# Kernel tuning notes

Measured on AMD Instinct MI355X. Metric: run time of the kernel, lower is better.

The kernel has to match this reference:

```python
import jax, jax.numpy as jnp
import numpy as np
from jax import lax

B, S, NX, NSFC, H, NY = 8192, 64, 4, 5, 32, 1


def _lstm(x, h0, c0, w_ih, w_hh, b_ih, b_hh):
    """batch_first LSTM, PyTorch gate order (i, f, g, o).
    x: [B,S,I]; h0,c0: [B,H]; w_ih: [4H,I]; w_hh: [4H,H]. Returns [B,S,H]."""
    # Precompute the input projection for all timesteps (big GEMM, once).
    xg = jnp.einsum('bsi,gi->bsg', x, w_ih) + b_ih + b_hh  # [B,S,4H]

    def step(carry, xg_t):
        h, c = carry
        gates = xg_t + h @ w_hh.T  # [B,4H]
        i, f, g, o = jnp.split(gates, 4, axis=-1)
        i = jax.nn.sigmoid(i)
        f = jax.nn.sigmoid(f)
        g = jnp.tanh(g)
        o = jax.nn.sigmoid(o)
        c = f * c + i * g
        h = o * jnp.tanh(c)
        return (h, c), h

    (_, _), hs = lax.scan(step, (h0, c0), jnp.swapaxes(xg, 0, 1))  # hs: [S,B,H]
    return jnp.swapaxes(hs, 0, 1)


def setup_inputs() -> dict:
    key = jax.random.key(0)
    ks = jax.random.split(key, 16)
    s = 1.0 / np.sqrt(H)

    def u(k, shape):
        return jax.random.uniform(k, shape, jnp.float32, -s, s)

    return {
        'inputs_main': jax.random.normal(ks[0], (B, S, NX), jnp.float32),
        'inputs_sfc': jax.random.normal(ks[1], (B, NSFC), jnp.float32),
        'w_sfc1': u(ks[2], (H, NSFC)), 'b_sfc1': u(ks[3], (H,)),
        'w_sfc2': u(ks[4], (H, NSFC)), 'b_sfc2': u(ks[5], (H,)),
        'w_ih1': u(ks[6], (4 * H, NX)), 'w_hh1': u(ks[7], (4 * H, H)),
        'b_ih1': u(ks[8], (4 * H,)), 'b_hh1': u(ks[9], (4 * H,)),
        'w_ih2': u(ks[10], (4 * H, H)), 'w_hh2': u(ks[11], (4 * H, H)),
        'b_ih2': u(ks[12], (4 * H,)), 'b_hh2': u(ks[13], (4 * H,)),
        'w_out': u(ks[14], (NY, H)), 'b_out': u(ks[15], (NY,)),
    }


def reference(inputs_main, inputs_sfc,
              w_sfc1, b_sfc1, w_sfc2, b_sfc2,
              w_ih1, w_hh1, b_ih1, b_hh1,
              w_ih2, w_hh2, b_ih2, b_hh2,
              w_out, b_out):
    # Surface MLPs -> initial (h0, c0) of rnn1
    h0 = jnp.tanh(inputs_sfc @ w_sfc1.T + b_sfc1)  # [B,H]
    c0 = jnp.tanh(inputs_sfc @ w_sfc2.T + b_sfc2)  # [B,H]

    # rnn1 runs on time-reversed input; its output is flipped back
    x = jnp.flip(inputs_main, axis=1)
    out = _lstm(x, h0, c0, w_ih1, w_hh1, b_ih1, b_hh1)
    out = jnp.flip(out, axis=1)

    # rnn2 with zero initial state (PyTorch default)
    z = jnp.zeros((out.shape[0], H), out.dtype)
    out2 = _lstm(out, z, z, w_ih2, w_hh2, b_ih2, b_hh2)

    # Output MLP (concat=False -> last layer output only)
    return out2 @ w_out.T + b_out  # [B,S,NY]
```

## Files before the change

kernel.cpp:

```cpp
#include <hip/hip_runtime.h>

typedef __attribute__((ext_vector_type(4))) float f32x4;
typedef __attribute__((ext_vector_type(8))) short bf16x8;

#define LOG2E 1.44269504088896340736f

__device__ __forceinline__ float bcf(unsigned u){ union{unsigned u;float f;}v; v.u=u; return v.f; }
__device__ __forceinline__ unsigned pkbf(float a, float b){
    unsigned w; asm("v_cvt_pk_bf16_f32 %0, %1, %2" : "=v"(w) : "v"(a), "v"(b)); return w;
}
__device__ __forceinline__ float ex2(float x){ return __builtin_amdgcn_exp2f(x); }
__device__ __forceinline__ float rcp_(float x){ return __builtin_amdgcn_rcpf(x); }

#define MFMA(a,b,c) __builtin_amdgcn_mfma_f32_16x16x32_bf16(a,b,c,0,0,0)

union FragU { unsigned w[4]; bf16x8 v; };

__device__ __forceinline__ void split8(const float* v, bf16x8 &fh, bf16x8 &fl){
    FragU H, L;
#pragma unroll
    for (int i=0;i<4;i++){
        unsigned w = pkbf(v[2*i], v[2*i+1]);
        H.w[i] = w;
        float ra = v[2*i]   - bcf(w<<16);
        float rb = v[2*i+1] - bcf(w & 0xffff0000u);
        L.w[i] = pkbf(ra, rb);
    }
    fh = H.v; fl = L.v;
}

__device__ __forceinline__ void build_bx(const float4& x, int hi, FragU& B){
    unsigned w0 = pkbf(x.x, x.y), w1 = pkbf(x.z, x.w);
    float r0 = x.x - bcf(w0<<16), r1 = x.y - bcf(w0 & 0xffff0000u);
    float r2 = x.z - bcf(w1<<16), r3 = x.w - bcf(w1 & 0xffff0000u);
    unsigned l0 = pkbf(r0,r1), l1 = pkbf(r2,r3);
    const bool h01 = (hi < 2);
    B.w[0] = h01 ? w0 : 0u;
    B.w[1] = h01 ? w1 : 0u;
    B.w[2] = (hi==0) ? l0 : (hi==1 ? 0x3f803f80u : 0u);
    B.w[3] = (hi==0) ? l1 : 0u;
}

__device__ __forceinline__ void write_h(unsigned (*hb)[16][20], int b15, int hi, int wv_,
                                        const float* hv){
    unsigned h0 = pkbf(hv[0], hv[1]);
    unsigned h1 = pkbf(hv[2], hv[3]);
    float r0 = hv[0]-bcf(h0<<16), r1 = hv[1]-bcf(h0 & 0xffff0000u);
    float r2 = hv[2]-bcf(h1<<16), r3 = hv[3]-bcf(h1 & 0xffff0000u);
    unsigned l0 = pkbf(r0,r1), l1 = pkbf(r2,r3);
    const int wi = 8*wv_ + 2*hi;
    *(uint2*)&hb[0][b15][wi] = make_uint2(h0,h1);
    *(uint2*)&hb[1][b15][wi] = make_uint2(l0,l1);
}

__global__ __launch_bounds__(128) void lstm2_mfma2(
    const float* __restrict__ xin,
    const float* __restrict__ sfc,
    const float* __restrict__ w_sfc1, const float* __restrict__ b_sfc1,
    const float* __restrict__ w_sfc2, const float* __restrict__ b_sfc2,
    const float* __restrict__ w_ih1, const float* __restrict__ w_hh1,
    const float* __restrict__ b_ih1, const float* __restrict__ b_hh1,
    const float* __restrict__ w_ih2, const float* __restrict__ w_hh2,
    const float* __restrict__ b_ih2, const float* __restrict__ b_hh2,
    const float* __restrict__ w_out, const float* __restrict__ b_out,
    float* __restrict__ outp)
{
    __shared__ __align__(16) unsigned out1q[64][16][16];
    __shared__ __align__(16) unsigned hbuf[2][2][16][20];
    __shared__ float ybuf[2][64][16];

    const int tid  = threadIdx.x;
    const int wv   = tid >> 6;
    const int lane = tid & 63;
    const int b15  = lane & 15;
    const int hi   = (lane >> 4) & 3;
    const int B0   = blockIdx.x * 16;

    bf16x8 Whh_h[4], Whh_l[4], WxA[4];
    bf16x8 W2h_h[4], W2h_l[4], W2x_h[4], W2x_l[4];
    float bia[4][4], woutr[4];
#pragma unroll
    for (int c=0;c<4;c++){
        const int gr = 32*c + 16*wv + b15;
        const float sc = (c==2) ? (2.0f*LOG2E) : (-LOG2E);
        float wvv[8];
        {
            float4 wa = *(const float4*)(w_hh1 + gr*32 + 8*hi);
            float4 wb = *(const float4*)(w_hh1 + gr*32 + 8*hi + 4);
            wvv[0]=wa.x*sc; wvv[1]=wa.y*sc; wvv[2]=wa.z*sc; wvv[3]=wa.w*sc;
            wvv[4]=wb.x*sc; wvv[5]=wb.y*sc; wvv[6]=wb.z*sc; wvv[7]=wb.w*sc;
        }
        split8(wvv, Whh_h[c], Whh_l[c]);
        {
            float4 wi = *(const float4*)(w_ih1 + gr*4);
            float wh0=wi.x*sc, wh1=wi.y*sc, wh2=wi.z*sc, wh3=wi.w*sc;
            unsigned xw0 = pkbf(wh0,wh1), xw1 = pkbf(wh2,wh3);
            float wl0 = wh0-bcf(xw0<<16), wl1 = wh1-bcf(xw0 & 0xffff0000u);
            float wl2 = wh2-bcf(xw1<<16), wl3 = wh3-bcf(xw1 & 0xffff0000u);
            unsigned lw0 = pkbf(wl0,wl1), lw1 = pkbf(wl2,wl3);
            float bias = (b_ih1[gr] + b_hh1[gr])*sc;
            unsigned bh = pkbf(bias, 0.0f);
            float blo = bias - bcf(bh<<16);
            unsigned bword = pkbf(bias, blo);
            FragU A;
            if (hi==0){ A.w[0]=xw0; A.w[1]=xw1; A.w[2]=xw0; A.w[3]=xw1; }
            else if (hi==1){ A.w[0]=lw0; A.w[1]=lw1; A.w[2]=bword; A.w[3]=0u; }
            else { A.w[0]=0u; A.w[1]=0u; A.w[2]=0u; A.w[3]=0u; }
            WxA[c] = A.v;
        }
        {
            float4 wa = *(const float4*)(w_hh2 + gr*32 + 8*hi);
            float4 wb = *(const float4*)(w_hh2 + gr*32 + 8*hi + 4);
            wvv[0]=wa.x*sc; wvv[1]=wa.y*sc; wvv[2]=wa.z*sc; wvv[3]=wa.w*sc;
            wvv[4]=wb.x*sc; wvv[5]=wb.y*sc; wvv[6]=wb.z*sc; wvv[7]=wb.w*sc;
        }
        split8(wvv, W2h_h[c], W2h_l[c]);
        {
            const float scx = sc * (1.0f/32767.0f);
            float4 wa = *(const float4*)(w_ih2 + gr*32 + 8*hi);
            float4 wb = *(const float4*)(w_ih2 + gr*32 + 8*hi + 4);
            wvv[0]=wa.x*scx; wvv[1]=wa.y*scx; wvv[2]=wa.z*scx; wvv[3]=wa.w*scx;
            wvv[4]=wb.x*scx; wvv[5]=wb.y*scx; wvv[6]=wb.z*scx; wvv[7]=wb.w*scx;
        }
        split8(wvv, W2x_h[c], W2x_l[c]);
    }
#pragma unroll
    for (int p=0;p<4;p++){
        const int j = 16*wv + 4*hi + p;
        bia[0][p] = (b_ih2[j]    + b_hh2[j])    * (-LOG2E);
        bia[1][p] = (b_ih2[32+j] + b_hh2[32+j]) * (-LOG2E);
        bia[2][p] = (b_ih2[64+j] + b_hh2[64+j]) * (2.0f*LOG2E);
        bia[3][p] = (b_ih2[96+j] + b_hh2[96+j]) * (-LOG2E);
        woutr[p]  = w_out[j];
    }

    float cs[4], hv[4];
    {
        const float* sp = sfc + (B0 + b15)*5;
        const float s0=sp[0], s1=sp[1], s2=sp[2], s3=sp[3], s4=sp[4];
#pragma unroll
        for (int p=0;p<4;p++){
            const int j = 16*wv + 4*hi + p;
            float a1 = b_sfc1[j] + s0*w_sfc1[j*5+0] + s1*w_sfc1[j*5+1]
                     + s2*w_sfc1[j*5+2] + s3*w_sfc1[j*5+3] + s4*w_sfc1[j*5+4];
            float a2 = b_sfc2[j] + s0*w_sfc2[j*5+0] + s1*w_sfc2[j*5+1]
                     + s2*w_sfc2[j*5+2] + s3*w_sfc2[j*5+3] + s4*w_sfc2[j*5+4];
            hv[p] = 1.0f - 2.0f*rcp_(ex2((2.0f*LOG2E)*a1)+1.0f);
            cs[p] = (2.0f*LOG2E)*(1.0f - 2.0f*rcp_(ex2((2.0f*LOG2E)*a2)+1.0f));
        }
    }
    write_h(hbuf[0], b15, hi, wv, hv);
    __syncthreads();

    int par = 0;
    FragU Bx;
    {
        float4 x0 = *(const float4*)(xin + ((B0 + b15)*64 + 63)*4);
        build_bx(x0, hi, Bx);
    }
#pragma unroll 1
    for (int t=63; t>=0; --t){
        bf16x8 Hh = *(const bf16x8*)&hbuf[par][0][b15][4*hi];
        bf16x8 Hl = *(const bf16x8*)&hbuf[par][1][b15][4*hi];
        f32x4 acc[4];
#pragma unroll
        for (int c=0;c<4;c++){
            f32x4 a = {0.f,0.f,0.f,0.f};
            a = MFMA(WxA[c],   Bx.v, a);
            a = MFMA(Whh_h[c], Hh,   a);
            a = MFMA(Whh_h[c], Hl,   a);
            a = MFMA(Whh_l[c], Hh,   a);
            acc[c] = a;
        }
        if (t){
            float4 xn = *(const float4*)(xin + ((B0 + b15)*64 + (t-1))*4);
            build_bx(xn, hi, Bx);
        }
        int q[4];
#pragma unroll
        for (int p=0;p<4;p++){
            float iv = acc[0][p], fv = acc[1][p], gv = acc[2][p], ov = acc[3][p];
            float si = rcp_(1.0f+ex2(iv));
            float sf = rcp_(1.0f+ex2(fv));
            float so = rcp_(1.0f+ex2(ov));
            float tg = 1.0f - 2.0f*rcp_(ex2(gv)+1.0f);
            cs[p] = fmaf(sf, cs[p], ((2.0f*LOG2E)*si)*tg);
            float tc = 1.0f - 2.0f*rcp_(ex2(cs[p])+1.0f);
            hv[p] = so*tc;
            q[p] = __float2int_rn(hv[p]*32767.0f);
        }
        unsigned q01 = ((unsigned)q[0] & 0xffffu) | ((unsigned)q[1] << 16);
        unsigned q23 = ((unsigned)q[2] & 0xffffu) | ((unsigned)q[3] << 16);
        *(uint2*)&out1q[t][b15][8*wv + 2*hi] = make_uint2(q01, q23);
        write_h(hbuf[par^1], b15, hi, wv, hv);
        __syncthreads();
        par ^= 1;
    }

    {
        const int wi = 8*wv + 2*hi;
        *(uint2*)&hbuf[par][0][b15][wi] = make_uint2(0u,0u);
        *(uint2*)&hbuf[par][1][b15][wi] = make_uint2(0u,0u);
        cs[0]=0.f; cs[1]=0.f; cs[2]=0.f; cs[3]=0.f;
    }
    FragU Xh, Xl;
    {
        const uint4 xw = *(const uint4*)&out1q[0][b15][4*hi];
        float xv[8];
        xv[0]=(float)(short)(xw.x & 0xffffu); xv[1]=(float)((int)xw.x >> 16);
        xv[2]=(float)(short)(xw.y & 0xffffu); xv[3]=(float)((int)xw.y >> 16);
        xv[4]=(float)(short)(xw.z & 0xffffu); xv[5]=(float)((int)xw.z >> 16);
        xv[6]=(float)(short)(xw.w & 0xffffu); xv[7]=(float)((int)xw.w >> 16);
        split8(xv, Xh.v, Xl.v);
    }
    __syncthreads();

#pragma unroll 1
    for (int t=0; t<64; ++t){
        bf16x8 Hh = *(const bf16x8*)&hbuf[par][0][b15][4*hi];
        bf16x8 Hl = *(const bf16x8*)&hbuf[par][1][b15][4*hi];
        f32x4 acc[4];
#pragma unroll
        for (int c=0;c<4;c++){
            f32x4 a = {0.f,0.f,0.f,0.f};
            a = MFMA(W2x_h[c], Xh.v, a);
            a = MFMA(W2x_h[c], Xl.v, a);
            a = MFMA(W2x_l[c], Xh.v, a);
            a = MFMA(W2h_h[c], Hh,   a);
            a = MFMA(W2h_h[c], Hl,   a);
            a = MFMA(W2h_l[c], Hh,   a);
            acc[c] = a;
        }
        const int tn = (t < 63) ? t+1 : 63;
        const uint4 xw = *(const uint4*)&out1q[tn][b15][4*hi];

        float y = 0.0f;
#pragma unroll
        for (int p=0;p<4;p++){
            float iv = acc[0][p] + bia[0][p];
            float fv = acc[1][p] + bia[1][p];
            float gv = acc[2][p] + bia[2][p];
            float ov = acc[3][p] + bia[3][p];
            float si = rcp_(1.0f+ex2(iv));
            float sf = rcp_(1.0f+ex2(fv));
            float so = rcp_(1.0f+ex2(ov));
            float tg = 1.0f - 2.0f*rcp_(ex2(gv)+1.0f);
            cs[p] = fmaf(sf, cs[p], ((2.0f*LOG2E)*si)*tg);
            float tc = 1.0f - 2.0f*rcp_(ex2(cs[p])+1.0f);
            hv[p] = so*tc;
            y = fmaf(hv[p], woutr[p], y);
        }
        y += __shfl_xor(y, 16, 64);
        y += __shfl_xor(y, 32, 64);
        if (hi == 0) ybuf[wv][t][b15] = y;
        write_h(hbuf[par^1], b15, hi, wv, hv);
        {
            float xv[8];
            xv[0]=(float)(short)(xw.x & 0xffffu); xv[1]=(float)((int)xw.x >> 16);
            xv[2]=(float)(short)(xw.y & 0xffffu); xv[3]=(float)((int)xw.y >> 16);
            xv[4]=(float)(short)(xw.z & 0xffffu); xv[5]=(float)((int)xw.z >> 16);
            xv[6]=(float)(short)(xw.w & 0xffffu); xv[7]=(float)((int)xw.w >> 16);
            split8(xv, Xh.v, Xl.v);
        }
        __syncthreads();
        par ^= 1;
    }

    const float bo = b_out[0];
    const int bb = tid >> 3;
    const int t0 = (tid & 7) * 8;
#pragma unroll
    for (int hlf=0; hlf<2; ++hlf){
        float4 v;
        v.x = ybuf[0][t0+4*hlf+0][bb] + ybuf[1][t0+4*hlf+0][bb] + bo;
        v.y = ybuf[0][t0+4*hlf+1][bb] + ybuf[1][t0+4*hlf+1][bb] + bo;
        v.z = ybuf[0][t0+4*hlf+2][bb] + ybuf[1][t0+4*hlf+2][bb] + bo;
        v.w = ybuf[0][t0+4*hlf+3][bb] + ybuf[1][t0+4*hlf+3][bb] + bo;
        *(float4*)(outp + (B0 + bb)*64 + t0 + 4*hlf) = v;
    }
}

extern "C" void kernel_launch(void* const* d_in, const int* in_sizes, int n_in,
                              void* d_out, int out_size, void* d_ws, size_t ws_size,
                              hipStream_t stream) {
    const float* xin    = (const float*)d_in[0];
    const float* sfc    = (const float*)d_in[1];
    const float* w_sfc1 = (const float*)d_in[2];
    const float* b_sfc1 = (const float*)d_in[3];
    const float* w_sfc2 = (const float*)d_in[4];
    const float* b_sfc2 = (const float*)d_in[5];
    const float* w_ih1  = (const float*)d_in[6];
    const float* w_hh1  = (const float*)d_in[7];
    const float* b_ih1  = (const float*)d_in[8];
    const float* b_hh1  = (const float*)d_in[9];
    const float* w_ih2  = (const float*)d_in[10];
    const float* w_hh2  = (const float*)d_in[11];
    const float* b_ih2  = (const float*)d_in[12];
    const float* b_hh2  = (const float*)d_in[13];
    const float* w_out  = (const float*)d_in[14];
    const float* b_out  = (const float*)d_in[15];
    float* out = (float*)d_out;

    dim3 grid(8192 / 16);
    dim3 block(128);
    hipLaunchKernelGGL(lstm2_mfma2, grid, block, 0, stream,
                       xin, sfc, w_sfc1, b_sfc1, w_sfc2, b_sfc2,
                       w_ih1, w_hh1, b_ih1, b_hh1,
                       w_ih2, w_hh2, b_ih2, b_hh2,
                       w_out, b_out, out);
}
```

Baseline: 175.1 us.

## Move layer-1 outputs to a global workspace and relax per-step barriers

The quantized layer-1 hidden states are now stored in a per-block global workspace instead of a 64 KB LDS array. Each step's __syncthreads is replaced by an LDS-only wait plus s_barrier, so outstanding global stores and loads no longer stall the recurrence. Input and workspace reads are prefetched two steps ahead so their latency overlaps with the MFMA and activation work. The trade is extra global traffic and a reliance on L2 hits for the second-layer reads, and the grid of 512 blocks may already be too small for the freed LDS to raise occupancy.

```diff
diff --git a/kernel.cpp b/kernel.cpp
--- a/kernel.cpp
+++ b/kernel.cpp
@@ -4,6 +4,7 @@
 typedef __attribute__((ext_vector_type(8))) short bf16x8;
 
 #define LOG2E 1.44269504088896340736f
+#define BAR_LGKM() asm volatile("s_waitcnt lgkmcnt(0)\n\ts_barrier" ::: "memory")
 
 __device__ __forceinline__ float bcf(unsigned u){ union{unsigned u;float f;}v; v.u=u; return v.f; }
 __device__ __forceinline__ unsigned pkbf(float a, float b){
@@ -41,19 +42,28 @@
     B.w[3] = (hi==0) ? l1 : 0u;
 }
 
-__device__ __forceinline__ void write_h(unsigned (*hb)[16][20], int b15, int hi, int wv_,
-                                        const float* hv){
-    unsigned h0 = pkbf(hv[0], hv[1]);
-    unsigned h1 = pkbf(hv[2], hv[3]);
-    float r0 = hv[0]-bcf(h0<<16), r1 = hv[1]-bcf(h0 & 0xffff0000u);
-    float r2 = hv[2]-bcf(h1<<16), r3 = hv[3]-bcf(h1 & 0xffff0000u);
+__device__ __forceinline__ void dec_q(const uint4& xw, FragU& Xh, FragU& Xl){
+    float xv[8];
+    xv[0]=(float)(short)(xw.x & 0xffffu); xv[1]=(float)((int)xw.x >> 16);
+    xv[2]=(float)(short)(xw.y & 0xffffu); xv[3]=(float)((int)xw.y >> 16);
+    xv[4]=(float)(short)(xw.z & 0xffffu); xv[5]=(float)((int)xw.z >> 16);
+    xv[6]=(float)(short)(xw.w & 0xffffu); xv[7]=(float)((int)xw.w >> 16);
+    split8(xv, Xh.v, Xl.v);
+}
+
+__device__ __forceinline__ void write_h_pair(unsigned (*hb)[16][20], int b15, int hi, int wv_,
+                                             const float* hvv){
+    unsigned h0 = pkbf(hvv[0], hvv[1]);
+    unsigned h1 = pkbf(hvv[2], hvv[3]);
+    float r0 = hvv[0]-bcf(h0<<16), r1 = hvv[1]-bcf(h0 & 0xffff0000u);
+    float r2 = hvv[2]-bcf(h1<<16), r3 = hvv[3]-bcf(h1 & 0xffff0000u);
     unsigned l0 = pkbf(r0,r1), l1 = pkbf(r2,r3);
     const int wi = 8*wv_ + 2*hi;
     *(uint2*)&hb[0][b15][wi] = make_uint2(h0,h1);
     *(uint2*)&hb[1][b15][wi] = make_uint2(l0,l1);
 }
 
-__global__ __launch_bounds__(128) void lstm2_mfma2(
+__global__ __launch_bounds__(128) void lstm2_g(
     const float* __restrict__ xin,
     const float* __restrict__ sfc,
     const float* __restrict__ w_sfc1, const float* __restrict__ b_sfc1,
@@ -63,9 +73,9 @@
     const float* __restrict__ w_ih2, const float* __restrict__ w_hh2,
     const float* __restrict__ b_ih2, const float* __restrict__ b_hh2,
     const float* __restrict__ w_out, const float* __restrict__ b_out,
-    float* __restrict__ outp)
+    float* __restrict__ outp,
+    unsigned* __restrict__ ws)
 {
-    __shared__ __align__(16) unsigned out1q[64][16][16];
     __shared__ __align__(16) unsigned hbuf[2][2][16][20];
     __shared__ float ybuf[2][64][16];
 
@@ -75,6 +85,7 @@
     const int b15  = lane & 15;
     const int hi   = (lane >> 4) & 3;
     const int B0   = blockIdx.x * 16;
+    unsigned* wsb  = ws + blockIdx.x * 16384;
 
     bf16x8 Whh_h[4], Whh_l[4], WxA[4];
     bf16x8 W2h_h[4], W2h_l[4], W2x_h[4], W2x_l[4];
@@ -134,7 +145,7 @@
         woutr[p]  = w_out[j];
     }
 
-    float cs[4], hv[4];
+    float cs[4], hvv[4];
     {
         const float* sp = sfc + (B0 + b15)*5;
         const float s0=sp[0], s1=sp[1], s2=sp[2], s3=sp[3], s4=sp[4];
@@ -145,21 +156,25 @@
                      + s2*w_sfc1[j*5+2] + s3*w_sfc1[j*5+3] + s4*w_sfc1[j*5+4];
             float a2 = b_sfc2[j] + s0*w_sfc2[j*5+0] + s1*w_sfc2[j*5+1]
                      + s2*w_sfc2[j*5+2] + s3*w_sfc2[j*5+3] + s4*w_sfc2[j*5+4];
-            hv[p] = 1.0f - 2.0f*rcp_(ex2((2.0f*LOG2E)*a1)+1.0f);
+            hvv[p] = 1.0f - 2.0f*rcp_(ex2((2.0f*LOG2E)*a1)+1.0f);
             cs[p] = (2.0f*LOG2E)*(1.0f - 2.0f*rcp_(ex2((2.0f*LOG2E)*a2)+1.0f));
         }
     }
-    write_h(hbuf[0], b15, hi, wv, hv);
+    write_h_pair(hbuf[0], b15, hi, wv, hvv);
     __syncthreads();
 
     int par = 0;
     FragU Bx;
+    float4 xraw;
     {
         float4 x0 = *(const float4*)(xin + ((B0 + b15)*64 + 63)*4);
         build_bx(x0, hi, Bx);
+        xraw = *(const float4*)(xin + ((B0 + b15)*64 + 62)*4);
     }
 #pragma unroll 1
     for (int t=63; t>=0; --t){
+        float4 xnext;
+        if (t >= 2) xnext = *(const float4*)(xin + ((B0 + b15)*64 + (t-2))*4);
         bf16x8 Hh = *(const bf16x8*)&hbuf[par][0][b15][4*hi];
         bf16x8 Hl = *(const bf16x8*)&hbuf[par][1][b15][4*hi];
         f32x4 acc[4];
@@ -171,10 +186,6 @@
             a = MFMA(Whh_h[c], Hl,   a);
             a = MFMA(Whh_l[c], Hh,   a);
             acc[c] = a;
-        }
-        if (t){
-            float4 xn = *(const float4*)(xin + ((B0 + b15)*64 + (t-1))*4);
-            build_bx(xn, hi, Bx);
         }
         int q[4];
 #pragma unroll
@@ -186,14 +197,16 @@
             float tg = 1.0f - 2.0f*rcp_(ex2(gv)+1.0f);
             cs[p] = fmaf(sf, cs[p], ((2.0f*LOG2E)*si)*tg);
             float tc = 1.0f - 2.0f*rcp_(ex2(cs[p])+1.0f);
-            hv[p] = so*tc;
-            q[p] = __float2int_rn(hv[p]*32767.0f);
+            hvv[p] = so*tc;
+            q[p] = __float2int_rn(hvv[p]*32767.0f);
         }
         unsigned q01 = ((unsigned)q[0] & 0xffffu) | ((unsigned)q[1] << 16);
         unsigned q23 = ((unsigned)q[2] & 0xffffu) | ((unsigned)q[3] << 16);
-        *(uint2*)&out1q[t][b15][8*wv + 2*hi] = make_uint2(q01, q23);
-        write_h(hbuf[par^1], b15, hi, wv, hv);
-        __syncthreads();
+        *(uint2*)&wsb[(t*16 + b15)*16 + 8*wv + 2*hi] = make_uint2(q01, q23);
+        write_h_pair(hbuf[par^1], b15, hi, wv, hvv);
+        if (t) build_bx(xraw, hi, Bx);
+        xraw = xnext;
+        BAR_LGKM();
         par ^= 1;
     }
 
@@ -203,20 +216,19 @@
         *(uint2*)&hbuf[par][1][b15][wi] = make_uint2(0u,0u);
         cs[0]=0.f; cs[1]=0.f; cs[2]=0.f; cs[3]=0.f;
     }
+    __syncthreads();
     FragU Xh, Xl;
+    uint4 xwraw;
     {
-        const uint4 xw = *(const uint4*)&out1q[0][b15][4*hi];
-        float xv[8];
-        xv[0]=(float)(short)(xw.x & 0xffffu); xv[1]=(float)((int)xw.x >> 16);
-        xv[2]=(float)(short)(xw.y & 0xffffu); xv[3]=(float)((int)xw.y >> 16);
-        xv[4]=(float)(short)(xw.z & 0xffffu); xv[5]=(float)((int)xw.z >> 16);
-        xv[6]=(float)(short)(xw.w & 0xffffu); xv[7]=(float)((int)xw.w >> 16);
-        split8(xv, Xh.v, Xl.v);
-    }
-    __syncthreads();
+        const uint4 xw0 = *(const uint4*)&wsb[(0*16 + b15)*16 + 4*hi];
+        dec_q(xw0, Xh, Xl);
+        xwraw = *(const uint4*)&wsb[(1*16 + b15)*16 + 4*hi];
+    }
 
 #pragma unroll 1
     for (int t=0; t<64; ++t){
+        const int tn2 = (t < 62) ? t+2 : 63;
+        const uint4 xwnext = *(const uint4*)&wsb[(tn2*16 + b15)*16 + 4*hi];
         bf16x8 Hh = *(const bf16x8*)&hbuf[par][0][b15][4*hi];
         bf16x8 Hl = *(const bf16x8*)&hbuf[par][1][b15][4*hi];
         f32x4 acc[4];
@@ -231,9 +243,6 @@
             a = MFMA(W2h_l[c], Hh,   a);
             acc[c] = a;
         }
-        const int tn = (t < 63) ? t+1 : 63;
-        const uint4 xw = *(const uint4*)&out1q[tn][b15][4*hi];
-
         float y = 0.0f;
 #pragma unroll
         for (int p=0;p<4;p++){
@@ -247,22 +256,16 @@
             float tg = 1.0f - 2.0f*rcp_(ex2(gv)+1.0f);
             cs[p] = fmaf(sf, cs[p], ((2.0f*LOG2E)*si)*tg);
             float tc = 1.0f - 2.0f*rcp_(ex2(cs[p])+1.0f);
-            hv[p] = so*tc;
-            y = fmaf(hv[p], woutr[p], y);
+            hvv[p] = so*tc;
+            y = fmaf(hvv[p], woutr[p], y);
         }
         y += __shfl_xor(y, 16, 64);
         y += __shfl_xor(y, 32, 64);
         if (hi == 0) ybuf[wv][t][b15] = y;
-        write_h(hbuf[par^1], b15, hi, wv, hv);
-        {
-            float xv[8];
-            xv[0]=(float)(short)(xw.x & 0xffffu); xv[1]=(float)((int)xw.x >> 16);
-            xv[2]=(float)(short)(xw.y & 0xffffu); xv[3]=(float)((int)xw.y >> 16);
-            xv[4]=(float)(short)(xw.z & 0xffffu); xv[5]=(float)((int)xw.z >> 16);
-            xv[6]=(float)(short)(xw.w & 0xffffu); xv[7]=(float)((int)xw.w >> 16);
-            split8(xv, Xh.v, Xl.v);
-        }
-        __syncthreads();
+        write_h_pair(hbuf[par^1], b15, hi, wv, hvv);
+        dec_q(xwraw, Xh, Xl);
+        xwraw = xwnext;
+        BAR_LGKM();
         par ^= 1;
     }
 
@@ -301,11 +304,9 @@
     const float* b_out  = (const float*)d_in[15];
     float* out = (float*)d_out;
 
-    dim3 grid(8192 / 16);
-    dim3 block(128);
-    hipLaunchKernelGGL(lstm2_mfma2, grid, block, 0, stream,
+    hipLaunchKernelGGL(lstm2_g, dim3(512), dim3(128), 0, stream,
                        xin, sfc, w_sfc1, b_sfc1, w_sfc2, b_sfc2,
                        w_ih1, w_hh1, b_ih1, b_hh1,
                        w_ih2, w_hh2, b_ih2, b_hh2,
-                       w_out, b_out, out);
-}
+                       w_out, b_out, out, (unsigned*)d_ws);
+}
```

Result: slower. 215.8 us (+23.2%).
